# Kernel optimization log

Measured on AMD Instinct MI355X. Metric: run time of the kernel, lower is better.

## Reference

```python
import jax, jax.numpy as jnp
import numpy as np

N_EMBD = 2048
NUM_GROUPS = 8
EXPERTS_PER_GROUP = 8
ROUTER_TEMPERATURE = 1.0
N_TOKENS = 16384


def setup_inputs() -> dict:
    key = jax.random.key(0)
    kx, kg, ke = jax.random.split(key, 3)
    x = jax.random.normal(kx, (N_TOKENS, N_EMBD), dtype=jnp.float32)
    # nn.Linear(in, out, bias=False) stores weight as [out, in]; kaiming-uniform-ish scale
    bound = 1.0 / np.sqrt(N_EMBD)
    group_gate_w = jax.random.uniform(kg, (NUM_GROUPS, N_EMBD), dtype=jnp.float32,
                                      minval=-bound, maxval=bound)
    expert_gate_w = jax.random.uniform(ke, (NUM_GROUPS * EXPERTS_PER_GROUP, N_EMBD),
                                       dtype=jnp.float32, minval=-bound, maxval=bound)
    return {"x": x, "group_gate_w": group_gate_w, "expert_gate_w": expert_gate_w}


def reference(x, group_gate_w, expert_gate_w):
    N = x.shape[0]
    G = NUM_GROUPS
    E_g = EXPERTS_PER_GROUP
    inv_temp = 1.0 / ROUTER_TEMPERATURE

    # Level 1: group routing
    group_logits = jnp.einsum('nd,gd->ng', x, group_gate_w)            # [N, G]
    group_probs = jax.nn.softmax(group_logits * inv_temp, axis=-1)     # [N, G]
    group_mask = group_probs >= (1.0 / G)                              # [N, G]

    # Level 2: expert routing within each group
    expert_logits = jnp.einsum('nd,ed->ne', x, expert_gate_w)          # [N, G*E_g]
    expert_logits = expert_logits.reshape(N, G, E_g)
    expert_probs = jax.nn.softmax(expert_logits * inv_temp, axis=-1)   # [N, G, E_g]
    expert_mask = expert_probs >= (1.0 / E_g)                          # [N, G, E_g]

    valid_mask_3d = group_mask[:, :, None] & expert_mask               # [N, G, E_g]
    selected_weights_3d = (group_probs[:, :, None] * expert_probs) * valid_mask_3d.astype(x.dtype)

    valid_mask = valid_mask_3d.reshape(N, G * E_g)
    selected_weights = selected_weights_3d.reshape(N, G * E_g)
    weight_sum = jnp.clip(jnp.sum(selected_weights, axis=-1, keepdims=True), 1e-9, None)
    normalized_weights = selected_weights / weight_sum
    return (valid_mask, normalized_weights)
```

## Files before the change

kernel.cpp:

```cpp
#include <hip/hip_runtime.h>
#include <hip/hip_bf16.h>


#define NT 16384
#define NE 2048
#define NCHUNK 32

#define QS 272
#define PL 1088
#define FP 2208
#define XB 22080
#define BUFSZ 30912
#define LDS_BYTES 61824

typedef _Float16 v8h __attribute__((ext_vector_type(8)));
typedef float    v4f __attribute__((ext_vector_type(4)));

__global__ __launch_bounds__(256)
void prep(const float* __restrict__ gw, const float* __restrict__ ew,
          float* __restrict__ Wbuf)
{
    const int u = blockIdx.x * 256 + threadIdx.x;
    const int g4 = u >> 12, gk = (u >> 6) & 63, q = (u >> 4) & 3, gr = u & 15;
    const int gate = g4 * 16 + gr;
    const int k = gk * 32 + q * 8;
    float v[8];
    if (gate < 64) {
        float4 a = *(const float4*)(ew + (size_t)gate * NE + k);
        float4 b = *(const float4*)(ew + (size_t)gate * NE + k + 4);
        v[0]=a.x; v[1]=a.y; v[2]=a.z; v[3]=a.w; v[4]=b.x; v[5]=b.y; v[6]=b.z; v[7]=b.w;
    } else if (gate < 72) {
        float4 a = *(const float4*)(gw + (size_t)(gate - 64) * NE + k);
        float4 b = *(const float4*)(gw + (size_t)(gate - 64) * NE + k + 4);
        v[0]=a.x; v[1]=a.y; v[2]=a.z; v[3]=a.w; v[4]=b.x; v[5]=b.y; v[6]=b.z; v[7]=b.w;
    } else {
        #pragma unroll
        for (int j = 0; j < 8; ++j) v[j] = 0.f;
    }
    v8h h, l;
    #pragma unroll
    for (int j = 0; j < 8; ++j) {
        _Float16 hh = (_Float16)v[j];
        h[j] = hh;
        l[j] = (_Float16)((v[j] - (float)hh) * 2048.0f);
    }
    char* p = (char*)Wbuf + (size_t)u * 32;
    *(v8h*)p        = h;
    *(v8h*)(p + 16) = l;
}

__global__ __launch_bounds__(512, 4)
void router(const float* __restrict__ x, const float* __restrict__ Wbuf,
            float* __restrict__ out)
{
    __shared__ __align__(16) char sm[LDS_BYTES];
    const int tid  = threadIdx.x;
    const int lane = tid & 63;
    const int w    = tid >> 6;
    const int t0   = blockIdx.x * 32;

    const char* w0src; int who0;
    {
        int g4 = tid >> 7, lks = (tid >> 6) & 1, q = (tid >> 4) & 3, gr = tid & 15;
        w0src = (const char*)Wbuf + (size_t)((((g4*64 + lks)*4 + q)*16 + gr) * 32);
        who0  = (g4*2 + lks)*FP + q*QS + gr*16;
    }
    const bool s1W = (tid < 128), s1X = (tid >= 128 && tid < 384);
    const char* w1src = nullptr; int who1 = 0;
    const float* xsrc = nullptr; int xho = 0;
    if (s1W) {
        int s = tid + 512;
        int g4 = s >> 7, lks = (s >> 6) & 1, q = (s >> 4) & 3, gr = s & 15;
        w1src = (const char*)Wbuf + (size_t)((((g4*64 + lks)*4 + q)*16 + gr) * 32);
        who1  = (g4*2 + lks)*FP + q*QS + gr*16;
    } else if (s1X) {
        int i2 = tid - 128;
        int q = i2 & 3, tr = (i2 >> 2) & 15, lks = (i2 >> 6) & 1, tt = (i2 >> 7) & 1;
        xsrc = x + (size_t)(t0 + tt*16 + tr) * NE + lks*32 + q*8;
        xho  = XB + (tt*2 + lks)*FP + q*QS + tr*16;
    }

    float4 wh0, wl0, wh1, wl1, xa, xb;
    auto stage_load = [&](int c) {
        const char* p0 = w0src + c * 4096;
        wh0 = *(const float4*)p0;  wl0 = *(const float4*)(p0 + 16);
        if (s1W) {
            const char* p1 = w1src + c * 4096;
            wh1 = *(const float4*)p1;  wl1 = *(const float4*)(p1 + 16);
        } else if (s1X) {
            xa = *(const float4*)(xsrc + c * 64);
            xb = *(const float4*)(xsrc + c * 64 + 4);
        }
    };
    auto stage_commit = [&](int buf) {
        const int bb = buf * BUFSZ;
        *(float4*)(sm + bb + who0)      = wh0;
        *(float4*)(sm + bb + who0 + PL) = wl0;
        if (s1W) {
            *(float4*)(sm + bb + who1)      = wh1;
            *(float4*)(sm + bb + who1 + PL) = wl1;
        } else if (s1X) {
            float v[8] = {xa.x, xa.y, xa.z, xa.w, xb.x, xb.y, xb.z, xb.w};
            v8h h, l;
            #pragma unroll
            for (int j = 0; j < 8; ++j) {
                _Float16 hh = (_Float16)v[j];
                h[j] = hh;
                l[j] = (_Float16)((v[j] - (float)hh) * 2048.0f);
            }
            *(v8h*)(sm + bb + xho)      = h;
            *(v8h*)(sm + bb + xho + PL) = l;
        }
    };

    const int tt = w & 1, s2 = (w >> 1) & 1, gh = w >> 2;
    const int ng = gh ? 2 : 3, gbase = gh ? 3 : 0;
    const int rdo = (lane >> 4) * QS + (lane & 15) * 16;

    v4f accHH[3], accC[3];
    #pragma unroll
    for (int g = 0; g < 3; ++g) { accHH[g] = (v4f)(0.f); accC[g] = (v4f)(0.f); }

    stage_load(0);
    stage_commit(0);
    for (int c = 0; c < NCHUNK; ++c) {
        if (c + 1 < NCHUNK) stage_load(c + 1);
        __syncthreads();
        {
            const int bb = (c & 1) * BUFSZ;
            const char* xbp = sm + bb + XB + (tt*2 + s2)*FP + rdo;
            v8h Bh = *(const v8h*)xbp;
            v8h Bl = *(const v8h*)(xbp + PL);
            #pragma unroll
            for (int gi = 0; gi < 3; ++gi) {
                if (gi < ng) {
                    const char* wbp = sm + bb + ((gbase + gi)*2 + s2)*FP + rdo;
                    v8h Ah = *(const v8h*)wbp;
                    v8h Al = *(const v8h*)(wbp + PL);
                    accHH[gi] = __builtin_amdgcn_mfma_f32_16x16x32_f16(Ah, Bh, accHH[gi], 0, 0, 0);
                    accC[gi]  = __builtin_amdgcn_mfma_f32_16x16x32_f16(Ah, Bl, accC[gi], 0, 0, 0);
                    accC[gi]  = __builtin_amdgcn_mfma_f32_16x16x32_f16(Al, Bh, accC[gi], 0, 0, 0);
                }
            }
        }
        if (c + 1 < NCHUNK) stage_commit((c + 1) & 1);
    }

    float part[3][4];
    #pragma unroll
    for (int gi = 0; gi < 3; ++gi)
        #pragma unroll
        for (int r = 0; r < 4; ++r)
            part[gi][r] = accHH[gi][r] + accC[gi][r] * (1.0f / 2048.0f);

    float* red = (float*)sm;
    if (s2 == 1) {
        #pragma unroll
        for (int gi = 0; gi < 3; ++gi)
            if (gi < ng)
                #pragma unroll
                for (int r = 0; r < 4; ++r)
                    red[((tt*5 + gbase + gi)*4 + r)*64 + lane] = part[gi][r];
    }
    __syncthreads();
    float* la = (float*)(sm + 12288);
    if (s2 == 0) {
        #pragma unroll
        for (int gi = 0; gi < 3; ++gi)
            if (gi < ng)
                #pragma unroll
                for (int r = 0; r < 4; ++r) {
                    float v = part[gi][r] + red[((tt*5 + gbase + gi)*4 + r)*64 + lane];
                    int gate  = (gbase + gi)*16 + (lane >> 4)*4 + r;
                    int token = tt*16 + (lane & 15);
                    la[token*80 + gate] = v;
                }
    }
    __syncthreads();

    if (tid < 32) {
        const float* lg = la + tid * 80;
        float* M = (float*)(sm + 24576) + tid * 64;
        float* W = (float*)(sm + 32768) + tid * 64;

        float gpb[8];
        float gmax = lg[64];
        #pragma unroll
        for (int g = 1; g < 8; ++g) gmax = fmaxf(gmax, lg[64 + g]);
        float gsum = 0.f;
        #pragma unroll
        for (int g = 0; g < 8; ++g) { gpb[g] = __expf(lg[64 + g] - gmax); gsum += gpb[g]; }
        const float ginv = 1.f / gsum;

        float sel[64];
        float wsum = 0.f;
        #pragma unroll
        for (int g = 0; g < 8; ++g) {
            const float gp_ = gpb[g] * ginv;
            float emax = lg[g * 8];
            #pragma unroll
            for (int j = 1; j < 8; ++j) emax = fmaxf(emax, lg[g * 8 + j]);
            float ep[8]; float esum = 0.f;
            #pragma unroll
            for (int j = 0; j < 8; ++j) { ep[j] = __expf(lg[g * 8 + j] - emax); esum += ep[j]; }
            const float einv = 1.f / esum;
            const bool gm = gp_ >= 0.125f;
            #pragma unroll
            for (int j = 0; j < 8; ++j) {
                const float pe = ep[j] * einv;
                const bool v = gm && (pe >= 0.125f);
                const float ww = v ? gp_ * pe : 0.f;
                M[g * 8 + j] = v ? 1.f : 0.f;
                sel[g * 8 + j] = ww;
                wsum += ww;
            }
        }
        const float inv = 1.f / fmaxf(wsum, 1e-9f);
        #pragma unroll
        for (int e = 0; e < 64; ++e) W[e] = sel[e] * inv;
    }
    __syncthreads();

    const float4* M4 = (const float4*)(sm + 24576);
    const float4* W4 = (const float4*)(sm + 32768);
    float4* o0 = (float4*)(out + (size_t)t0 * 64);
    float4* o1 = (float4*)(out + (size_t)NT * 64 + (size_t)t0 * 64);
    o0[tid] = M4[tid];
    o1[tid] = W4[tid];
}

extern "C" void kernel_launch(void* const* d_in, const int* in_sizes, int n_in,
                              void* d_out, int out_size, void* d_ws, size_t ws_size,
                              hipStream_t stream) {
    const float* x  = (const float*)d_in[0];
    const float* gw = (const float*)d_in[1];
    const float* ew = (const float*)d_in[2];
    float* out  = (float*)d_out;
    float* Wbuf = (float*)d_ws;

    prep<<<dim3(80),  dim3(256), 0, stream>>>(gw, ew, Wbuf);
    router<<<dim3(NT / 32), dim3(512), 0, stream>>>(x, Wbuf, out);
}
```

Measured before the change: 231.9 us.

## Stream x and weights directly into registers with split-K across waves

The router kernel no longer stages x and weights through double-buffered LDS with per-chunk barriers. Each wave now loads its x fragments and the prepacked fp16 hi/lo weights straight from global memory into registers, and handles 32 tokens by 80 gates over a quarter of the K dimension. Partial sums are combined with a two-step LDS reduction at the end. Blocks now cover 64 tokens instead of 32 and allow 2 blocks per CU instead of 4. This removes the per-chunk barriers and LDS traffic, at the cost of more registers, lower occupancy, and weight reloads from L2 in every wave.

```diff
diff --git a/kernel.cpp b/kernel.cpp
--- a/kernel.cpp
+++ b/kernel.cpp
@@ -4,14 +4,6 @@
 
 #define NT 16384
 #define NE 2048
-#define NCHUNK 32
-
-#define QS 272
-#define PL 1088
-#define FP 2208
-#define XB 22080
-#define BUFSZ 30912
-#define LDS_BYTES 61824
 
 typedef _Float16 v8h __attribute__((ext_vector_type(8)));
 typedef float    v4f __attribute__((ext_vector_type(4)));
@@ -49,139 +41,129 @@
     *(v8h*)(p + 16) = l;
 }
 
-__global__ __launch_bounds__(512, 4)
+#define P_BASE  0
+#define LA_BASE 10240
+#define M_BASE  15424
+#define W_BASE  19520
+#define SM_FLOATS 23616
+
+__global__ __launch_bounds__(512, 2)
 void router(const float* __restrict__ x, const float* __restrict__ Wbuf,
             float* __restrict__ out)
 {
-    __shared__ __align__(16) char sm[LDS_BYTES];
+    __shared__ __align__(16) float sm[SM_FLOATS];
     const int tid  = threadIdx.x;
     const int lane = tid & 63;
     const int w    = tid >> 6;
-    const int t0   = blockIdx.x * 32;
-
-    const char* w0src; int who0;
-    {
-        int g4 = tid >> 7, lks = (tid >> 6) & 1, q = (tid >> 4) & 3, gr = tid & 15;
-        w0src = (const char*)Wbuf + (size_t)((((g4*64 + lks)*4 + q)*16 + gr) * 32);
-        who0  = (g4*2 + lks)*FP + q*QS + gr*16;
-    }
-    const bool s1W = (tid < 128), s1X = (tid >= 128 && tid < 384);
-    const char* w1src = nullptr; int who1 = 0;
-    const float* xsrc = nullptr; int xho = 0;
-    if (s1W) {
-        int s = tid + 512;
-        int g4 = s >> 7, lks = (s >> 6) & 1, q = (s >> 4) & 3, gr = s & 15;
-        w1src = (const char*)Wbuf + (size_t)((((g4*64 + lks)*4 + q)*16 + gr) * 32);
-        who1  = (g4*2 + lks)*FP + q*QS + gr*16;
-    } else if (s1X) {
-        int i2 = tid - 128;
-        int q = i2 & 3, tr = (i2 >> 2) & 15, lks = (i2 >> 6) & 1, tt = (i2 >> 7) & 1;
-        xsrc = x + (size_t)(t0 + tt*16 + tr) * NE + lks*32 + q*8;
-        xho  = XB + (tt*2 + lks)*FP + q*QS + tr*16;
-    }
-
-    float4 wh0, wl0, wh1, wl1, xa, xb;
-    auto stage_load = [&](int c) {
-        const char* p0 = w0src + c * 4096;
-        wh0 = *(const float4*)p0;  wl0 = *(const float4*)(p0 + 16);
-        if (s1W) {
-            const char* p1 = w1src + c * 4096;
-            wh1 = *(const float4*)p1;  wl1 = *(const float4*)(p1 + 16);
-        } else if (s1X) {
-            xa = *(const float4*)(xsrc + c * 64);
-            xb = *(const float4*)(xsrc + c * 64 + 4);
-        }
-    };
-    auto stage_commit = [&](int buf) {
-        const int bb = buf * BUFSZ;
-        *(float4*)(sm + bb + who0)      = wh0;
-        *(float4*)(sm + bb + who0 + PL) = wl0;
-        if (s1W) {
-            *(float4*)(sm + bb + who1)      = wh1;
-            *(float4*)(sm + bb + who1 + PL) = wl1;
-        } else if (s1X) {
-            float v[8] = {xa.x, xa.y, xa.z, xa.w, xb.x, xb.y, xb.z, xb.w};
+    const int s2   = w >> 1;
+    const int th   = w & 1;
+    const int t0   = blockIdx.x * 64;
+    const int n    = lane & 15;
+    const int q    = lane >> 4;
+
+    const float* xr0 = x + (size_t)(t0 + th * 32 + n) * NE + s2 * 512 + q * 8;
+    const float* xr1 = xr0 + (size_t)16 * NE;
+    const char* wbp = (const char*)Wbuf;
+    const int   wlo = q * 512 + n * 32;
+
+    v4f aHH[2][5], aC[2][5];
+    #pragma unroll
+    for (int ti = 0; ti < 2; ++ti)
+        #pragma unroll
+        for (int g = 0; g < 5; ++g) { aHH[ti][g] = (v4f)(0.f); aC[ti][g] = (v4f)(0.f); }
+
+    float4 xc[2][2], xn[2][2];
+    xc[0][0] = *(const float4*)(xr0);      xc[0][1] = *(const float4*)(xr0 + 4);
+    xc[1][0] = *(const float4*)(xr1);      xc[1][1] = *(const float4*)(xr1 + 4);
+
+    for (int j = 0; j < 16; ++j) {
+        const int gk = s2 * 16 + j;
+        v8h Wh[5], Wl[5];
+        #pragma unroll
+        for (int g = 0; g < 5; ++g) {
+            const char* p = wbp + (size_t)(g * 64 + gk) * 2048 + wlo;
+            Wh[g] = *(const v8h*)p;
+            Wl[g] = *(const v8h*)(p + 16);
+        }
+        if (j + 1 < 16) {
+            const float* p0 = xr0 + (j + 1) * 32;
+            const float* p1 = xr1 + (j + 1) * 32;
+            xn[0][0] = *(const float4*)p0;  xn[0][1] = *(const float4*)(p0 + 4);
+            xn[1][0] = *(const float4*)p1;  xn[1][1] = *(const float4*)(p1 + 4);
+        }
+        v8h Bh[2], Bl[2];
+        #pragma unroll
+        for (int ti = 0; ti < 2; ++ti) {
+            float v[8] = {xc[ti][0].x, xc[ti][0].y, xc[ti][0].z, xc[ti][0].w,
+                          xc[ti][1].x, xc[ti][1].y, xc[ti][1].z, xc[ti][1].w};
             v8h h, l;
             #pragma unroll
-            for (int j = 0; j < 8; ++j) {
-                _Float16 hh = (_Float16)v[j];
-                h[j] = hh;
-                l[j] = (_Float16)((v[j] - (float)hh) * 2048.0f);
+            for (int e = 0; e < 8; ++e) {
+                _Float16 hh = (_Float16)v[e];
+                h[e] = hh;
+                l[e] = (_Float16)((v[e] - (float)hh) * 2048.0f);
             }
-            *(v8h*)(sm + bb + xho)      = h;
-            *(v8h*)(sm + bb + xho + PL) = l;
-        }
-    };
-
-    const int tt = w & 1, s2 = (w >> 1) & 1, gh = w >> 2;
-    const int ng = gh ? 2 : 3, gbase = gh ? 3 : 0;
-    const int rdo = (lane >> 4) * QS + (lane & 15) * 16;
-
-    v4f accHH[3], accC[3];
+            Bh[ti] = h; Bl[ti] = l;
+        }
+        #pragma unroll
+        for (int g = 0; g < 5; ++g) {
+            #pragma unroll
+            for (int ti = 0; ti < 2; ++ti) {
+                aHH[ti][g] = __builtin_amdgcn_mfma_f32_16x16x32_f16(Wh[g], Bh[ti], aHH[ti][g], 0, 0, 0);
+                aC[ti][g]  = __builtin_amdgcn_mfma_f32_16x16x32_f16(Wh[g], Bl[ti], aC[ti][g], 0, 0, 0);
+                aC[ti][g]  = __builtin_amdgcn_mfma_f32_16x16x32_f16(Wl[g], Bh[ti], aC[ti][g], 0, 0, 0);
+            }
+        }
+        #pragma unroll
+        for (int ti = 0; ti < 2; ++ti) { xc[ti][0] = xn[ti][0]; xc[ti][1] = xn[ti][1]; }
+    }
+
+    v4f part[2][5];
     #pragma unroll
-    for (int g = 0; g < 3; ++g) { accHH[g] = (v4f)(0.f); accC[g] = (v4f)(0.f); }
-
-    stage_load(0);
-    stage_commit(0);
-    for (int c = 0; c < NCHUNK; ++c) {
-        if (c + 1 < NCHUNK) stage_load(c + 1);
-        __syncthreads();
-        {
-            const int bb = (c & 1) * BUFSZ;
-            const char* xbp = sm + bb + XB + (tt*2 + s2)*FP + rdo;
-            v8h Bh = *(const v8h*)xbp;
-            v8h Bl = *(const v8h*)(xbp + PL);
-            #pragma unroll
-            for (int gi = 0; gi < 3; ++gi) {
-                if (gi < ng) {
-                    const char* wbp = sm + bb + ((gbase + gi)*2 + s2)*FP + rdo;
-                    v8h Ah = *(const v8h*)wbp;
-                    v8h Al = *(const v8h*)(wbp + PL);
-                    accHH[gi] = __builtin_amdgcn_mfma_f32_16x16x32_f16(Ah, Bh, accHH[gi], 0, 0, 0);
-                    accC[gi]  = __builtin_amdgcn_mfma_f32_16x16x32_f16(Ah, Bl, accC[gi], 0, 0, 0);
-                    accC[gi]  = __builtin_amdgcn_mfma_f32_16x16x32_f16(Al, Bh, accC[gi], 0, 0, 0);
-                }
-            }
-        }
-        if (c + 1 < NCHUNK) stage_commit((c + 1) & 1);
-    }
-
-    float part[3][4];
-    #pragma unroll
-    for (int gi = 0; gi < 3; ++gi)
-        #pragma unroll
-        for (int r = 0; r < 4; ++r)
-            part[gi][r] = accHH[gi][r] + accC[gi][r] * (1.0f / 2048.0f);
-
-    float* red = (float*)sm;
-    if (s2 == 1) {
-        #pragma unroll
-        for (int gi = 0; gi < 3; ++gi)
-            if (gi < ng)
+    for (int ti = 0; ti < 2; ++ti)
+        #pragma unroll
+        for (int g = 0; g < 5; ++g) {
+            v4f p;
+            #pragma unroll
+            for (int r = 0; r < 4; ++r) p[r] = aHH[ti][g][r] + aC[ti][g][r] * (1.0f / 2048.0f);
+            part[ti][g] = p;
+        }
+
+    float4* P4 = (float4*)(sm + P_BASE);
+    #define WRITE_P(slot) { _Pragma("unroll") for (int ti = 0; ti < 2; ++ti)          \
+        _Pragma("unroll") for (int g = 0; g < 5; ++g) {                               \
+            v4f p = part[ti][g];                                                      \
+            P4[((ti * 5 + g) * 4 + (slot)) * 64 + lane] = make_float4(p[0],p[1],p[2],p[3]); } }
+    #define ADD_P(slot) { _Pragma("unroll") for (int ti = 0; ti < 2; ++ti)            \
+        _Pragma("unroll") for (int g = 0; g < 5; ++g) {                               \
+            float4 v = P4[((ti * 5 + g) * 4 + (slot)) * 64 + lane];                   \
+            part[ti][g][0] += v.x; part[ti][g][1] += v.y;                             \
+            part[ti][g][2] += v.z; part[ti][g][3] += v.w; } }
+
+    if (s2 & 1) WRITE_P((s2 >> 1) * 2 + th);
+    __syncthreads();
+    if (!(s2 & 1)) ADD_P((s2 >> 1) * 2 + th);
+    __syncthreads();
+    if (s2 == 2) WRITE_P(2 + th);
+    __syncthreads();
+    if (s2 == 0) ADD_P(2 + th);
+
+    float* la = sm + LA_BASE;
+    if (s2 == 0) {
+        #pragma unroll
+        for (int ti = 0; ti < 2; ++ti)
+            #pragma unroll
+            for (int g = 0; g < 5; ++g)
                 #pragma unroll
                 for (int r = 0; r < 4; ++r)
-                    red[((tt*5 + gbase + gi)*4 + r)*64 + lane] = part[gi][r];
-    }
-    __syncthreads();
-    float* la = (float*)(sm + 12288);
-    if (s2 == 0) {
-        #pragma unroll
-        for (int gi = 0; gi < 3; ++gi)
-            if (gi < ng)
-                #pragma unroll
-                for (int r = 0; r < 4; ++r) {
-                    float v = part[gi][r] + red[((tt*5 + gbase + gi)*4 + r)*64 + lane];
-                    int gate  = (gbase + gi)*16 + (lane >> 4)*4 + r;
-                    int token = tt*16 + (lane & 15);
-                    la[token*80 + gate] = v;
-                }
-    }
-    __syncthreads();
-
-    if (tid < 32) {
-        const float* lg = la + tid * 80;
-        float* M = (float*)(sm + 24576) + tid * 64;
-        float* W = (float*)(sm + 32768) + tid * 64;
+                    la[(th * 32 + ti * 16 + n) * 81 + g * 16 + q * 4 + r] = part[ti][g][r];
+    }
+    __syncthreads();
+
+    if (tid < 64) {
+        const float* lg = la + tid * 81;
+        float* M = sm + M_BASE + tid * 64;
+        float* W = sm + W_BASE + tid * 64;
 
         float gpb[8];
         float gmax = lg[64];
@@ -221,12 +203,17 @@
     }
     __syncthreads();
 
-    const float4* M4 = (const float4*)(sm + 24576);
-    const float4* W4 = (const float4*)(sm + 32768);
+    const float4* M4 = (const float4*)(sm + M_BASE);
+    const float4* W4 = (const float4*)(sm + W_BASE);
     float4* o0 = (float4*)(out + (size_t)t0 * 64);
     float4* o1 = (float4*)(out + (size_t)NT * 64 + (size_t)t0 * 64);
-    o0[tid] = M4[tid];
-    o1[tid] = W4[tid];
+    o0[tid]       = M4[tid];
+    o0[tid + 512] = M4[tid + 512];
+    o1[tid]       = W4[tid];
+    o1[tid + 512] = W4[tid + 512];
+
+    #undef WRITE_P
+    #undef ADD_P
 }
 
 extern "C" void kernel_launch(void* const* d_in, const int* in_sizes, int n_in,
@@ -238,6 +225,6 @@
     float* out  = (float*)d_out;
     float* Wbuf = (float*)d_ws;
 
-    prep<<<dim3(80),  dim3(256), 0, stream>>>(gw, ew, Wbuf);
-    router<<<dim3(NT / 32), dim3(512), 0, stream>>>(x, Wbuf, out);
+    prep<<<dim3(80),   dim3(256), 0, stream>>>(gw, ew, Wbuf);
+    router<<<dim3(NT / 64), dim3(512), 0, stream>>>(x, Wbuf, out);
 }
```

New measurement: 218.7 us. 1.06x faster.
